# Performance work log

Hardware: AMD Instinct MI355X
Metric: run time of the kernel (lower is better)

Reference implementation:

```python
import jax, jax.numpy as jnp
import numpy as np

N_NODES = 50000
N_EDGES = 3200000
N_GRAPHS = 50
IN_FEATS, HIDDEN, OUT_FEATS = 5, 64, 2


def setup_inputs() -> dict:
    key = jax.random.key(0)
    ks = jax.random.split(key, 10)
    x = jax.random.normal(ks[0], (N_NODES, IN_FEATS), dtype=jnp.float32)
    edge_index = jax.random.randint(ks[1], (2, N_EDGES), 0, N_NODES, dtype=jnp.int64)
    edge_attr = jax.random.uniform(ks[2], (N_EDGES, 1), dtype=jnp.float32)
    batch = jnp.sort(jax.random.randint(ks[3], (N_NODES,), 0, N_GRAPHS, dtype=jnp.int64))
    s1 = 1.0 / np.sqrt(IN_FEATS)
    s2 = 1.0 / np.sqrt(HIDDEN)
    W1 = jax.random.uniform(ks[4], (IN_FEATS, HIDDEN), jnp.float32, -s1, s1)
    b1 = jnp.zeros((HIDDEN,), jnp.float32)
    W2 = jax.random.uniform(ks[5], (HIDDEN, HIDDEN), jnp.float32, -s2, s2)
    b2 = jnp.zeros((HIDDEN,), jnp.float32)
    Wo = jax.random.uniform(ks[6], (HIDDEN, OUT_FEATS), jnp.float32, -s2, s2)
    bo = jax.random.uniform(ks[7], (OUT_FEATS,), jnp.float32, -s2, s2)
    return {"x": x, "edge_index": edge_index, "edge_attr": edge_attr, "batch": batch,
            "W1": W1, "b1": b1, "W2": W2, "b2": b2, "Wo": Wo, "bo": bo}


def _gcn_conv(x, src, dst, ew, W, b):
    # symmetric normalization: D^{-1/2} (A + I) D^{-1/2}, weighted degrees
    deg = jax.ops.segment_sum(ew, dst, num_segments=N_NODES)
    dinv = jnp.where(deg > 0, jax.lax.rsqrt(jnp.where(deg > 0, deg, 1.0)), 0.0)
    norm = dinv[src] * ew * dinv[dst]  # [E+N]
    h = x @ W                           # transform before propagate (PyG order)
    msg = h[src] * norm[:, None]        # gather + scale per edge
    out = jax.ops.segment_sum(msg, dst, num_segments=N_NODES)
    return out + b


def reference(x, edge_index, edge_attr, batch, W1, b1, W2, b2, Wo, bo):
    ew = edge_attr.squeeze(-1)
    loop = jnp.arange(N_NODES, dtype=edge_index.dtype)  # add self-loops (GCNConv default)
    src = jnp.concatenate([edge_index[0], loop])
    dst = jnp.concatenate([edge_index[1], loop])
    ew = jnp.concatenate([ew, jnp.ones((N_NODES,), ew.dtype)])
    h = jax.nn.relu(_gcn_conv(x, src, dst, ew, W1, b1))
    h = jax.nn.relu(_gcn_conv(h, src, dst, ew, W2, b2))
    # global mean pool over graphs
    sums = jax.ops.segment_sum(h, batch, num_segments=N_GRAPHS)
    cnt = jax.ops.segment_sum(jnp.ones((N_NODES,), h.dtype), batch, num_segments=N_GRAPHS)
    pooled = sums / jnp.maximum(cnt, 1.0)[:, None]
    return pooled @ Wo + bo  # [N_GRAPHS, OUT_FEATS]
```

## Files before the change

### kernel.cpp

```cpp
#include <hip/hip_runtime.h>
#include <hip/hip_fp16.h>

#define N_NODES 50000
#define N_EDGES 3200000
#define N_GRAPHS 50
#define IN_F 5
#define HID 64
#define OUT_F 2

#define BKT_SHIFT 5
#define BKT_W 32
#define NBKT 1563
#define NB1 250
#define EPB 12800
#define CAP 2560
#define TILE_SHIFT 12
#define NBIN (BKT_W * 16)
#define NWAVE 8192

__global__ void k_bhist(const int* dst, unsigned short* cw) {
    __shared__ int hist[NBKT];
    int t = threadIdx.x, blk = blockIdx.x;
    for (int b = t; b < NBKT; b += 1024) hist[b] = 0;
    __syncthreads();
    int base = blk * EPB;
    for (int k = t; k < EPB; k += 1024)
        atomicAdd(&hist[dst[base + k] >> BKT_SHIFT], 1);
    __syncthreads();
    for (int b = t; b < NBKT; b += 1024)
        cw[b * NB1 + blk] = (unsigned short)hist[b];
}

__global__ void k_bscanA(unsigned short* cw, int* total) {
    __shared__ int s[256];
    int t = threadIdx.x, b = blockIdx.x;
    int v = (t < NB1) ? (int)cw[b * NB1 + t] : 0;
    s[t] = v;
    __syncthreads();
    for (int off = 1; off < 256; off <<= 1) {
        int a = (t >= off) ? s[t - off] : 0;
        __syncthreads();
        s[t] += a;
        __syncthreads();
    }
    if (t < NB1) cw[b * NB1 + t] = (unsigned short)(s[t] - v);
    if (t == 255) total[b] = s[255];
}

__global__ void k_bscanB(const int* total, int* rpB) {
    __shared__ int s[256];
    int t = threadIdx.x;
    int v[7], sum = 0;
#pragma unroll
    for (int j = 0; j < 7; ++j) {
        int idx = t * 7 + j;
        v[j] = (idx < NBKT) ? total[idx] : 0;
        sum += v[j];
    }
    s[t] = sum;
    __syncthreads();
    for (int off = 1; off < 256; off <<= 1) {
        int a = (t >= off) ? s[t - off] : 0;
        __syncthreads();
        s[t] += a;
        __syncthreads();
    }
    int run = s[t] - sum;
#pragma unroll
    for (int j = 0; j < 7; ++j) {
        int idx = t * 7 + j;
        if (idx < NBKT) rpB[idx] = run;
        run += v[j];
    }
    if (t == 0) rpB[NBKT] = N_EDGES;
}

__global__ void k_bucket(const int* src, const int* dst, const float* ew,
                         const unsigned short* cw, const int* rpB, int* bkt) {
    __shared__ int base[NBKT];
    __shared__ int off[NBKT];
    int t = threadIdx.x, blk = blockIdx.x;
    for (int b = t; b < NBKT; b += 1024) {
        base[b] = (int)cw[b * NB1 + blk] + rpB[b];
        off[b] = 0;
    }
    __syncthreads();
    int ebase = blk * EPB;
    for (int k = t; k < EPB; k += 1024) {
        int idx = ebase + k;
        int d = dst[idx];
        int b = d >> BKT_SHIFT;
        int sl = base[b] + atomicAdd(&off[b], 1);
        int wq = (int)rintf(ew[idx] * 2047.0f);
        bkt[sl] = src[idx] | ((d & (BKT_W - 1)) << 16) | (wq << 21);
    }
}

__global__ void k_bsort(const int* rpB, int* bkt, int* rp2, int* rp2e, float* dinv) {
    __shared__ int ebuf[CAP];
    __shared__ int hist[NBIN];
    __shared__ int binoff[NBIN];
    __shared__ int s[256];
    __shared__ int wdI[BKT_W];
    int t = threadIdx.x, b = blockIdx.x;
    int e0 = rpB[b], cnt = rpB[b + 1] - e0;
    for (int i = t; i < NBIN; i += 256) hist[i] = 0;
    if (t < BKT_W) wdI[t] = 0;
    __syncthreads();
    for (int k = t; k < cnt; k += 256) {
        int u = bkt[e0 + k];
        ebuf[k] = u;
        int dl = (u >> 16) & (BKT_W - 1);
        int bin = (dl << 4) | ((u & 0xFFFF) >> TILE_SHIFT);
        atomicAdd(&hist[bin], 1);
        atomicAdd(&wdI[dl], (int)((unsigned)u >> 21));
    }
    __syncthreads();
    int h0 = hist[2 * t], h1 = hist[2 * t + 1];
    int pv = h0 + h1;
    s[t] = pv;
    __syncthreads();
    for (int off = 1; off < 256; off <<= 1) {
        int a = (t >= off) ? s[t - off] : 0;
        __syncthreads();
        s[t] += a;
        __syncthreads();
    }
    int pe = s[t] - pv;
    binoff[2 * t] = pe;
    binoff[2 * t + 1] = pe + h0;
    __syncthreads();
    if (t < BKT_W) {
        int node = (b << BKT_SHIFT) + t;
        if (node < N_NODES) {
            int startl = binoff[t << 4];
            int endl = (t == BKT_W - 1) ? cnt : binoff[(t + 1) << 4];
            rp2[node]  = e0 + startl;
            rp2e[node] = e0 + endl;
            dinv[node] = rsqrtf(1.0f + (float)wdI[t] * (1.0f / 2047.0f));
        }
    }
    __syncthreads();
    for (int k = t; k < cnt; k += 256) {
        int u = ebuf[k];
        int dl = (u >> 16) & (BKT_W - 1);
        int bin = (dl << 4) | ((u & 0xFFFF) >> TILE_SHIFT);
        int pos = atomicAdd(&binoff[bin], 1);
        float wf = (float)((unsigned)u >> 21) * (1.0f / 2047.0f);
        unsigned short wh = __half_as_ushort(__float2half(wf));
        bkt[e0 + pos] = (u & 0xFFFF) | ((int)wh << 16);
    }
}

__global__ void k_xprep(const float* x, const float* dinv, __half* xp) {
    int i = blockIdx.x * 256 + threadIdx.x;
    if (i < N_NODES) {
        float di = dinv[i];
        const float* xi = &x[i * IN_F];
        __half* o = &xp[i * 8];
#pragma unroll
        for (int f = 0; f < IN_F; ++f) o[f] = __float2half(xi[f] * di);
        o[5] = o[6] = o[7] = __float2half(0.f);
    }
}

__global__ void k_p(const int* rp2, const int* rp2e, const int* pk,
                    const __half* xp, const float* dinv, float* p) {
    int node = blockIdx.x * 4 + (threadIdx.x >> 6);
    int lane = threadIdx.x & 63;
    if (node >= N_NODES) return;
    int b = rp2[node], en = rp2e[node];
    float a0 = 0.f, a1 = 0.f, a2 = 0.f, a3 = 0.f, a4 = 0.f;
    for (int k = b + lane; k < en; k += 64) {
        int e = pk[k];
        float w = __half2float(__ushort_as_half((unsigned short)((unsigned)e >> 16)));
        const __half* xs = &xp[(e & 0xFFFF) * 8];
        int4 xv = *reinterpret_cast<const int4*>(xs);
        __half2 p01 = *(__half2*)&xv.x;
        __half2 p23 = *(__half2*)&xv.y;
        __half2 p45 = *(__half2*)&xv.z;
        a0 += w * __half2float(p01.x); a1 += w * __half2float(p01.y);
        a2 += w * __half2float(p23.x); a3 += w * __half2float(p23.y);
        a4 += w * __half2float(p45.x);
    }
    for (int off = 32; off; off >>= 1) {
        a0 += __shfl_down(a0, off); a1 += __shfl_down(a1, off); a2 += __shfl_down(a2, off);
        a3 += __shfl_down(a3, off); a4 += __shfl_down(a4, off);
    }
    if (lane == 0) {
        float di = dinv[node];
        const __half* xn = &xp[node * 8];
        float* pp = &p[node * IN_F];
        pp[0] = di * (a0 + __half2float(xn[0]));
        pp[1] = di * (a1 + __half2float(xn[1]));
        pp[2] = di * (a2 + __half2float(xn[2]));
        pp[3] = di * (a3 + __half2float(xn[3]));
        pp[4] = di * (a4 + __half2float(xn[4]));
    }
}

__global__ void k_h1g(const float* p, const float* W1, const float* b1,
                      const float* W2, const float* dinv,
                      unsigned char* g8u, float* rs) {
    __shared__ float W1s[IN_F * HID];
    __shared__ float W2s[HID * HID];
    __shared__ float b1s[HID];
    int t = threadIdx.x;
    for (int k = t; k < IN_F * HID; k += 256) W1s[k] = W1[k];
    for (int k = t; k < HID * HID; k += 256) W2s[k] = W2[k];
    if (t < HID) b1s[t] = b1[t];
    __syncthreads();
    int lane = t & 63;
    int wid = blockIdx.x * 4 + (t >> 6);
    int nw = gridDim.x * 4;
    for (int node = wid; node < N_NODES; node += nw) {
        const float* pp = &p[node * IN_F];
        float pv0 = pp[0], pv1 = pp[1], pv2 = pp[2], pv3 = pp[3], pv4 = pp[4];
        float h = b1s[lane] + pv0 * W1s[lane] + pv1 * W1s[64 + lane] + pv2 * W1s[128 + lane]
                + pv3 * W1s[192 + lane] + pv4 * W1s[256 + lane];
        h = fmaxf(h, 0.f);
        float acc = 0.f;
#pragma unroll
        for (int f = 0; f < HID; ++f) {
            float hf = __int_as_float(__builtin_amdgcn_readlane(__float_as_int(h), f));
            acc += hf * W2s[f * HID + lane];
        }
        float gv = acc * dinv[node];
        float am = fabsf(gv);
        for (int off = 32; off; off >>= 1) am = fmaxf(am, __shfl_xor(am, off));
        float inv = (am > 0.f) ? 127.0f / am : 0.f;
        g8u[node * HID + lane] = (unsigned char)(__float2int_rn(gv * inv) + 128);
        if (lane == 0) rs[node] = (am > 0.f) ? am * (1.0f / 127.0f) : 0.f;
    }
}

#define EDGE4_BODY(UU)                                                         \
    {                                                                          \
        int u_ = (UU);                                                         \
        float w_ = __half2float(__ushort_as_half((unsigned short)((unsigned)u_ >> 16))); \
        float wwv_ = w_ * rs[u_ & 0xFFFF];                                     \
        unsigned dw_ = *(const unsigned*)&g8u[(u_ & 0xFFFF) * HID + fo];       \
        a0 += wwv_ * (float)(dw_ & 0xFF);                                      \
        a1 += wwv_ * (float)((dw_ >> 8) & 0xFF);                               \
        a2 += wwv_ * (float)((dw_ >> 16) & 0xFF);                              \
        a3 += wwv_ * (float)(dw_ >> 24);                                       \
        sww += wwv_;                                                           \
    }

__global__ __launch_bounds__(256, 8) void k_h2g(const int* rp2, const int* rp2e,
                      const int* pk, const float* dinv, const unsigned char* g8u,
                      const float* rs, const float* b2, const int* batch, float* pool) {
    int t = threadIdx.x, lane = t & 63;
    int grp = lane >> 4;
    int fo = (lane & 15) << 2;
    int wid = blockIdx.x * 4 + (t >> 6);
    int n0 = (int)(((long long)wid * N_NODES) / NWAVE);
    int n1 = (int)(((long long)(wid + 1) * N_NODES) / NWAVE);
    if (n0 >= n1) return;
    float4 bj = *reinterpret_cast<const float4*>(&b2[fo]);
    float p0 = 0.f, p1 = 0.f, p2 = 0.f, p3 = 0.f;
    int cur = batch[n0];
    for (int node = n0; node < n1; ++node) {
        unsigned dws = *(const unsigned*)&g8u[node * HID + fo];
        float wq4 = 0.25f * rs[node];
        float a0 = wq4 * (float)(dws & 0xFF);
        float a1 = wq4 * (float)((dws >> 8) & 0xFF);
        float a2 = wq4 * (float)((dws >> 16) & 0xFF);
        float a3 = wq4 * (float)(dws >> 24);
        float sww = wq4;
        for (int k0 = rp2[node], e1 = rp2e[node]; k0 < e1; k0 += 64) {
            int kk = k0 + lane;
            int ev = (kk < e1) ? pk[kk] : 0;
            int m = e1 - k0; if (m > 64) m = 64;
            if (m == 64) {
#pragma unroll
                for (int q = 0; q < 16; ++q) EDGE4_BODY(__shfl(ev, (q << 2) | grp))
            } else {
                int ng = (m + 3) >> 2;
                for (int q = 0; q < ng; ++q) EDGE4_BODY(__shfl(ev, (q << 2) | grp))
            }
        }
#pragma unroll
        for (int off = 16; off <= 32; off <<= 1) {
            a0 += __shfl_xor(a0, off); a1 += __shfl_xor(a1, off);
            a2 += __shfl_xor(a2, off); a3 += __shfl_xor(a3, off);
            sww += __shfl_xor(sww, off);
        }
        float di = dinv[node];
        float corr = 128.0f * sww;
        float h0 = fmaxf(di * (a0 - corr) + bj.x, 0.f);
        float h1 = fmaxf(di * (a1 - corr) + bj.y, 0.f);
        float h2 = fmaxf(di * (a2 - corr) + bj.z, 0.f);
        float h3 = fmaxf(di * (a3 - corr) + bj.w, 0.f);
        int bb = batch[node];
        if (bb != cur) {
            if (lane < 16) {
                float* pb = &pool[cur * HID + fo];
                atomicAdd(pb + 0, p0); atomicAdd(pb + 1, p1);
                atomicAdd(pb + 2, p2); atomicAdd(pb + 3, p3);
            }
            cur = bb;
            p0 = p1 = p2 = p3 = 0.f;
        }
        p0 += h0; p1 += h1; p2 += h2; p3 += h3;
    }
    if (lane < 16) {
        float* pb = &pool[cur * HID + fo];
        atomicAdd(pb + 0, p0); atomicAdd(pb + 1, p1);
        atomicAdd(pb + 2, p2); atomicAdd(pb + 3, p3);
    }
}

__device__ int lowb(const int* a, int n, int v) {
    int lo = 0, hi = n;
    while (lo < hi) { int m = (lo + hi) >> 1; if (a[m] < v) lo = m + 1; else hi = m; }
    return lo;
}

__global__ void k_out(const float* pool, const int* batch, const float* Wo,
                      const float* bo, float* out) {
    int t = blockIdx.x * blockDim.x + threadIdx.x;
    if (t < N_GRAPHS * OUT_F) {
        int gi = t / OUT_F, k = t % OUT_F;
        int c = lowb(batch, N_NODES, gi + 1) - lowb(batch, N_NODES, gi);
        float cf = fmaxf((float)c, 1.0f);
        float acc = bo[k];
        for (int f = 0; f < HID; ++f)
            acc += (pool[gi * HID + f] / cf) * Wo[f * OUT_F + k];
        out[t] = acc;
    }
}

extern "C" void kernel_launch(void* const* d_in, const int* in_sizes, int n_in,
                              void* d_out, int out_size, void* d_ws, size_t ws_size,
                              hipStream_t stream) {
    const float* x   = (const float*)d_in[0];
    const int*   ei  = (const int*)d_in[1];
    const float* ea  = (const float*)d_in[2];
    const int*   bat = (const int*)d_in[3];
    const float* W1  = (const float*)d_in[4];
    const float* b1  = (const float*)d_in[5];
    const float* W2  = (const float*)d_in[6];
    const float* b2  = (const float*)d_in[7];
    const float* Wo  = (const float*)d_in[8];
    const float* bo  = (const float*)d_in[9];
    float* out = (float*)d_out;

    const int* src = ei;
    const int* dst = ei + N_EDGES;

    float* ws = (float*)d_ws;
    int*   rpB   = (int*)ws;
    int*   rp2   = (int*)(ws + 1568);
    int*   rp2e  = (int*)(ws + 51584);
    float* dinv  = ws + 101600;
    float* rs    = ws + 151616;
    float* pool  = ws + 201632;
    int*   total = (int*)(ws + 201632);
    unsigned short* cw = (unsigned short*)(ws + 204832);
    float* p     = ws + 204832;
    int*   bkt   = (int*)(ws + 454832);
    unsigned char* g8u = (unsigned char*)(ws + 3654832);
    __half* xp   = (__half*)(ws + 4454832);

    k_bhist <<<NB1, 1024, 0, stream>>>(dst, cw);
    k_bscanA<<<NBKT, 256, 0, stream>>>(cw, total);
    k_bscanB<<<1, 256, 0, stream>>>(total, rpB);
    hipMemsetAsync(pool, 0, N_GRAPHS * HID * sizeof(float), stream);
    k_bucket<<<NB1, 1024, 0, stream>>>(src, dst, ea, cw, rpB, bkt);
    k_bsort <<<NBKT, 256, 0, stream>>>(rpB, bkt, rp2, rp2e, dinv);
    k_xprep <<<(N_NODES + 255) / 256, 256, 0, stream>>>(x, dinv, xp);
    k_p     <<<(N_NODES + 3) / 4, 256, 0, stream>>>(rp2, rp2e, bkt, xp, dinv, p);
    k_h1g   <<<1024, 256, 0, stream>>>(p, W1, b1, W2, dinv, g8u, rs);
    k_h2g   <<<NWAVE / 4, 256, 0, stream>>>(rp2, rp2e, bkt, dinv, g8u, rs, b2, bat, pool);
    k_out   <<<1, 128, 0, stream>>>(pool, bat, Wo, bo, out);
}
```

Measured before the change: 279.8 us.

## Widen dst buckets to 128 nodes, drop source tiling, fuse xprep into sort

Buckets for the counting sort grow from 32 to 128 destination nodes, so there are fewer, larger blocks (1024 threads). Within a bucket, edges are now sorted only by destination, not by source tile. Edge weights move from an 11-bit quantised field into a separate fp16 array, and degrees are accumulated with float atomics. The xprep kernel is folded into the sort kernel. This removes one launch and shrinks the histogram and scan work, but drops the source-tile ordering that helped gather locality in the aggregation kernels, adds an extra 2-byte-per-edge stream, and CAP2 of 9216 may overflow for heavy buckets (about 8192 edges on average).

```diff
diff --git a/kernel.cpp b/kernel.cpp
--- a/kernel.cpp
+++ b/kernel.cpp
@@ -8,26 +8,25 @@
 #define HID 64
 #define OUT_F 2
 
-#define BKT_SHIFT 5
-#define BKT_W 32
-#define NBKT 1563
+#define BK2_SHIFT 7
+#define BK2_W 128
+#define NBKT2 391
 #define NB1 250
 #define EPB 12800
-#define CAP 2560
-#define TILE_SHIFT 12
-#define NBIN (BKT_W * 16)
+#define CAP2 9216
+#define NBIN2 128
 #define NWAVE 8192
 
 __global__ void k_bhist(const int* dst, unsigned short* cw) {
-    __shared__ int hist[NBKT];
+    __shared__ int hist[NBKT2];
     int t = threadIdx.x, blk = blockIdx.x;
-    for (int b = t; b < NBKT; b += 1024) hist[b] = 0;
+    for (int b = t; b < NBKT2; b += 1024) hist[b] = 0;
     __syncthreads();
     int base = blk * EPB;
     for (int k = t; k < EPB; k += 1024)
-        atomicAdd(&hist[dst[base + k] >> BKT_SHIFT], 1);
-    __syncthreads();
-    for (int b = t; b < NBKT; b += 1024)
+        atomicAdd(&hist[dst[base + k] >> BK2_SHIFT], 1);
+    __syncthreads();
+    for (int b = t; b < NBKT2; b += 1024)
         cw[b * NB1 + blk] = (unsigned short)hist[b];
 }
 
@@ -50,11 +49,11 @@
 __global__ void k_bscanB(const int* total, int* rpB) {
     __shared__ int s[256];
     int t = threadIdx.x;
-    int v[7], sum = 0;
-#pragma unroll
-    for (int j = 0; j < 7; ++j) {
-        int idx = t * 7 + j;
-        v[j] = (idx < NBKT) ? total[idx] : 0;
+    int v[2], sum = 0;
+#pragma unroll
+    for (int j = 0; j < 2; ++j) {
+        int idx = t * 2 + j;
+        v[j] = (idx < NBKT2) ? total[idx] : 0;
         sum += v[j];
     }
     s[t] = sum;
@@ -67,20 +66,21 @@
     }
     int run = s[t] - sum;
 #pragma unroll
-    for (int j = 0; j < 7; ++j) {
-        int idx = t * 7 + j;
-        if (idx < NBKT) rpB[idx] = run;
+    for (int j = 0; j < 2; ++j) {
+        int idx = t * 2 + j;
+        if (idx < NBKT2) rpB[idx] = run;
         run += v[j];
     }
-    if (t == 0) rpB[NBKT] = N_EDGES;
+    if (t == 0) rpB[NBKT2] = N_EDGES;
 }
 
 __global__ void k_bucket(const int* src, const int* dst, const float* ew,
-                         const unsigned short* cw, const int* rpB, int* bkt) {
-    __shared__ int base[NBKT];
-    __shared__ int off[NBKT];
+                         const unsigned short* cw, const int* rpB,
+                         int* key4, unsigned short* wh2) {
+    __shared__ int base[NBKT2];
+    __shared__ int off[NBKT2];
     int t = threadIdx.x, blk = blockIdx.x;
-    for (int b = t; b < NBKT; b += 1024) {
+    for (int b = t; b < NBKT2; b += 1024) {
         base[b] = (int)cw[b * NB1 + blk] + rpB[b];
         off[b] = 0;
     }
@@ -89,78 +89,64 @@
     for (int k = t; k < EPB; k += 1024) {
         int idx = ebase + k;
         int d = dst[idx];
-        int b = d >> BKT_SHIFT;
+        int b = d >> BK2_SHIFT;
         int sl = base[b] + atomicAdd(&off[b], 1);
-        int wq = (int)rintf(ew[idx] * 2047.0f);
-        bkt[sl] = src[idx] | ((d & (BKT_W - 1)) << 16) | (wq << 21);
-    }
-}
-
-__global__ void k_bsort(const int* rpB, int* bkt, int* rp2, int* rp2e, float* dinv) {
-    __shared__ int ebuf[CAP];
-    __shared__ int hist[NBIN];
-    __shared__ int binoff[NBIN];
-    __shared__ int s[256];
-    __shared__ int wdI[BKT_W];
+        key4[sl] = src[idx] | ((d & (BK2_W - 1)) << 16);
+        wh2[sl] = __half_as_ushort(__float2half(ew[idx]));
+    }
+}
+
+__global__ __launch_bounds__(1024) void k_bsort2(const int* rpB, int* key4,
+                      const unsigned short* wh2, const float* x,
+                      int* rp2, int* rp2e, float* dinv, __half* xp) {
+    __shared__ int keybuf[CAP2];
+    __shared__ unsigned short whbuf[CAP2];
+    __shared__ int hist[NBIN2];
+    __shared__ int binoff[NBIN2];
+    __shared__ int s[NBIN2];
+    __shared__ float wd[NBIN2];
     int t = threadIdx.x, b = blockIdx.x;
     int e0 = rpB[b], cnt = rpB[b + 1] - e0;
-    for (int i = t; i < NBIN; i += 256) hist[i] = 0;
-    if (t < BKT_W) wdI[t] = 0;
-    __syncthreads();
-    for (int k = t; k < cnt; k += 256) {
-        int u = bkt[e0 + k];
-        ebuf[k] = u;
-        int dl = (u >> 16) & (BKT_W - 1);
-        int bin = (dl << 4) | ((u & 0xFFFF) >> TILE_SHIFT);
-        atomicAdd(&hist[bin], 1);
-        atomicAdd(&wdI[dl], (int)((unsigned)u >> 21));
-    }
-    __syncthreads();
-    int h0 = hist[2 * t], h1 = hist[2 * t + 1];
-    int pv = h0 + h1;
-    s[t] = pv;
-    __syncthreads();
-    for (int off = 1; off < 256; off <<= 1) {
-        int a = (t >= off) ? s[t - off] : 0;
-        __syncthreads();
-        s[t] += a;
-        __syncthreads();
-    }
-    int pe = s[t] - pv;
-    binoff[2 * t] = pe;
-    binoff[2 * t + 1] = pe + h0;
-    __syncthreads();
-    if (t < BKT_W) {
-        int node = (b << BKT_SHIFT) + t;
+    if (t < NBIN2) { hist[t] = 0; wd[t] = 0.f; }
+    __syncthreads();
+    for (int k = t; k < cnt; k += 1024) {
+        int u = key4[e0 + k];
+        unsigned short wh = wh2[e0 + k];
+        keybuf[k] = u; whbuf[k] = wh;
+        int dl = (u >> 16) & (BK2_W - 1);
+        atomicAdd(&hist[dl], 1);
+        atomicAdd(&wd[dl], __half2float(__ushort_as_half(wh)));
+    }
+    __syncthreads();
+    if (t < NBIN2) s[t] = hist[t];
+    __syncthreads();
+    for (int off = 1; off < NBIN2; off <<= 1) {
+        int a = (t < NBIN2 && t >= off) ? s[t - off] : 0;
+        __syncthreads();
+        if (t < NBIN2) s[t] += a;
+        __syncthreads();
+    }
+    if (t < NBIN2) {
+        binoff[t] = s[t] - hist[t];
+        int node = (b << BK2_SHIFT) + t;
         if (node < N_NODES) {
-            int startl = binoff[t << 4];
-            int endl = (t == BKT_W - 1) ? cnt : binoff[(t + 1) << 4];
-            rp2[node]  = e0 + startl;
-            rp2e[node] = e0 + endl;
-            dinv[node] = rsqrtf(1.0f + (float)wdI[t] * (1.0f / 2047.0f));
-        }
-    }
-    __syncthreads();
-    for (int k = t; k < cnt; k += 256) {
-        int u = ebuf[k];
-        int dl = (u >> 16) & (BKT_W - 1);
-        int bin = (dl << 4) | ((u & 0xFFFF) >> TILE_SHIFT);
-        int pos = atomicAdd(&binoff[bin], 1);
-        float wf = (float)((unsigned)u >> 21) * (1.0f / 2047.0f);
-        unsigned short wh = __half_as_ushort(__float2half(wf));
-        bkt[e0 + pos] = (u & 0xFFFF) | ((int)wh << 16);
-    }
-}
-
-__global__ void k_xprep(const float* x, const float* dinv, __half* xp) {
-    int i = blockIdx.x * 256 + threadIdx.x;
-    if (i < N_NODES) {
-        float di = dinv[i];
-        const float* xi = &x[i * IN_F];
-        __half* o = &xp[i * 8];
-#pragma unroll
-        for (int f = 0; f < IN_F; ++f) o[f] = __float2half(xi[f] * di);
-        o[5] = o[6] = o[7] = __float2half(0.f);
+            rp2[node]  = e0 + s[t] - hist[t];
+            rp2e[node] = e0 + s[t];
+            float di = rsqrtf(1.0f + wd[t]);
+            dinv[node] = di;
+            const float* xi = &x[node * IN_F];
+            __half* o = &xp[node * 8];
+#pragma unroll
+            for (int f = 0; f < IN_F; ++f) o[f] = __float2half(xi[f] * di);
+            o[5] = o[6] = o[7] = __float2half(0.f);
+        }
+    }
+    __syncthreads();
+    for (int k = t; k < cnt; k += 1024) {
+        int u = keybuf[k];
+        int dl = (u >> 16) & (BK2_W - 1);
+        int pos = atomicAdd(&binoff[dl], 1);
+        key4[e0 + pos] = (u & 0xFFFF) | ((int)whbuf[k] << 16);
     }
 }
 
@@ -351,27 +337,27 @@
 
     float* ws = (float*)d_ws;
     int*   rpB   = (int*)ws;
-    int*   rp2   = (int*)(ws + 1568);
-    int*   rp2e  = (int*)(ws + 51584);
-    float* dinv  = ws + 101600;
-    float* rs    = ws + 151616;
-    float* pool  = ws + 201632;
-    int*   total = (int*)(ws + 201632);
-    unsigned short* cw = (unsigned short*)(ws + 204832);
-    float* p     = ws + 204832;
-    int*   bkt   = (int*)(ws + 454832);
-    unsigned char* g8u = (unsigned char*)(ws + 3654832);
-    __half* xp   = (__half*)(ws + 4454832);
+    int*   rp2   = (int*)(ws + 400);
+    int*   rp2e  = (int*)(ws + 50416);
+    float* dinv  = ws + 100432;
+    float* rs    = ws + 150448;
+    float* pool  = ws + 200464;
+    int*   total = (int*)(ws + 200464);
+    float* p     = ws + 203664;
+    unsigned short* cw = (unsigned short*)(ws + 203664);
+    int*   key4  = (int*)(ws + 453664);
+    unsigned short* wh2 = (unsigned short*)(ws + 3653664);
+    unsigned char* g8u = (unsigned char*)(ws + 5253664);
+    __half* xp   = (__half*)(ws + 6053664);
 
     k_bhist <<<NB1, 1024, 0, stream>>>(dst, cw);
-    k_bscanA<<<NBKT, 256, 0, stream>>>(cw, total);
+    k_bscanA<<<NBKT2, 256, 0, stream>>>(cw, total);
     k_bscanB<<<1, 256, 0, stream>>>(total, rpB);
     hipMemsetAsync(pool, 0, N_GRAPHS * HID * sizeof(float), stream);
-    k_bucket<<<NB1, 1024, 0, stream>>>(src, dst, ea, cw, rpB, bkt);
-    k_bsort <<<NBKT, 256, 0, stream>>>(rpB, bkt, rp2, rp2e, dinv);
-    k_xprep <<<(N_NODES + 255) / 256, 256, 0, stream>>>(x, dinv, xp);
-    k_p     <<<(N_NODES + 3) / 4, 256, 0, stream>>>(rp2, rp2e, bkt, xp, dinv, p);
+    k_bucket<<<NB1, 1024, 0, stream>>>(src, dst, ea, cw, rpB, key4, wh2);
+    k_bsort2<<<NBKT2, 1024, 0, stream>>>(rpB, key4, wh2, x, rp2, rp2e, dinv, xp);
+    k_p     <<<(N_NODES + 3) / 4, 256, 0, stream>>>(rp2, rp2e, key4, xp, dinv, p);
     k_h1g   <<<1024, 256, 0, stream>>>(p, W1, b1, W2, dinv, g8u, rs);
-    k_h2g   <<<NWAVE / 4, 256, 0, stream>>>(rp2, rp2e, bkt, dinv, g8u, rs, b2, bat, pool);
+    k_h2g   <<<NWAVE / 4, 256, 0, stream>>>(rp2, rp2e, key4, dinv, g8u, rs, b2, bat, pool);
     k_out   <<<1, 128, 0, stream>>>(pool, bat, Wo, bo, out);
 }
```

Result: slower. 305.2 us (+9.1%).
